# Kernel optimization log

Measured on AMD Instinct MI355X. Metric: run time of the kernel, lower is better.

The kernel has to match this reference:

```python
import jax, jax.numpy as jnp
import numpy as np


def setup_inputs() -> dict:
    key = jax.random.key(0)
    k1, k2, k3, k4, k5 = jax.random.split(key, 5)
    N, T, D, H = 256, 64, 1024, 1024
    x = jax.random.normal(k1, (N, T, D), dtype=jnp.float32)
    A = jax.random.normal(k2, (N, H, 4, 4), dtype=jnp.float32)
    Wx = jax.random.normal(k3, (D, 4 * H), dtype=jnp.float32) / np.sqrt(D)
    Wh = jax.random.normal(k4, (H, 4 * H), dtype=jnp.float32) / np.sqrt(H)
    Wattn = jax.random.normal(k5, (H, 4 * H), dtype=jnp.float32) / np.sqrt(H)
    b = jnp.zeros((4 * H,), dtype=jnp.float32)
    return {"x": x, "A": A, "Wx": Wx, "Wh": Wh, "Wattn": Wattn, "b": b}


def reference(x, A, Wx, Wh, Wattn, b):
    N, T, D = x.shape
    H = A.shape[1]
    A_flat = A.reshape(N, H, 16)           # (N, H, 16) flattened 4x4 grid
    scale = 1.0 / jnp.sqrt(jnp.asarray(H, dtype=x.dtype))

    h0 = A.mean(axis=(2, 3))               # (N, H)
    c0 = h0

    def step(carry, xt):
        prev_h, prev_c = carry
        # scaled dot-product attention over the 16 spatial locations
        scores = jnp.einsum('nh,nhl->nl', prev_h, A_flat) * scale  # (N, 16)
        w = jax.nn.softmax(scores, axis=1)
        attn = jnp.einsum('nhl,nl->nh', A_flat, w)                 # (N, H)
        # fused LSTM gate pre-activation
        a = xt @ Wx + prev_h @ Wh + attn @ Wattn + b               # (N, 4H)
        ai, af, ao, ag = jnp.split(a, 4, axis=1)
        i = jax.nn.sigmoid(ai)
        f = jax.nn.sigmoid(af)
        o = jax.nn.sigmoid(ao)
        g = jnp.tanh(ag)
        next_c = f * prev_c + i * g
        next_h = o * jnp.tanh(next_c)
        return (next_h, next_c), next_h

    xs = jnp.swapaxes(x, 0, 1)             # (T, N, D)
    _, hs = jax.lax.scan(step, (h0, c0), xs)
    return jnp.swapaxes(hs, 0, 1)          # (N, T, H)
```

## Files before the change

kernel.cpp:

```cpp
#include <hip/hip_runtime.h>

typedef _Float16 f16;
typedef _Float16 f16x2 __attribute__((ext_vector_type(2)));
typedef _Float16 f16x4 __attribute__((ext_vector_type(4)));
typedef _Float16 f16x8 __attribute__((ext_vector_type(8)));
typedef float f32x4 __attribute__((ext_vector_type(4)));

#define N_ 256
#define T_ 64
#define D_ 1024
#define H_ 1024
#define K3 3072
#define G4 4096

__global__ void k_transpose(const float* __restrict__ Wx, const float* __restrict__ Wh,
                            const float* __restrict__ Wattn, f16* __restrict__ W3T) {
    __shared__ float tile[32][33];
    int j0 = blockIdx.x * 32;
    int k0 = blockIdx.y * 32;
    int tx = threadIdx.x;
    int ty = threadIdx.y;
    for (int i = 0; i < 4; i++) {
        int k = k0 + ty + i * 8;
        const float* W = (k < 1024) ? Wx : ((k < 2048) ? Wh : Wattn);
        int kr = k & 1023;
        tile[ty + i * 8][tx] = W[(size_t)kr * 4096 + j0 + tx];
    }
    __syncthreads();
    for (int i = 0; i < 4; i++) {
        int j = j0 + ty + i * 8;
        W3T[(size_t)j * K3 + k0 + tx] = (f16)tile[tx][ty + i * 8];
    }
}

__global__ void k_castA(const float* __restrict__ A, f16* __restrict__ A16) {
    int i = blockIdx.x * 256 + threadIdx.x;
    float4 v = ((const float4*)A)[i];
    f16x4 h4 = {(f16)v.x, (f16)v.y, (f16)v.z, (f16)v.w};
    ((f16x4*)A16)[i] = h4;
}

__global__ void k_castX(const float* __restrict__ x, f16* __restrict__ x16) {
    size_t i = (size_t)blockIdx.x * 2048 + (size_t)threadIdx.x * 8;
    float4 v0 = *(const float4*)(x + i);
    float4 v1 = *(const float4*)(x + i + 4);
    f16x8 h;
    h[0] = (f16)v0.x; h[1] = (f16)v0.y; h[2] = (f16)v0.z; h[3] = (f16)v0.w;
    h[4] = (f16)v1.x; h[5] = (f16)v1.y; h[6] = (f16)v1.z; h[7] = (f16)v1.w;
    *(f16x8*)(x16 + i) = h;
}

__global__ void k_castAT(const float* __restrict__ A, f16* __restrict__ AT16) {
    __shared__ f16 sA[16 * 1024];
    int n = blockIdx.x;
    int tid = threadIdx.x;
    for (int i = 0; i < 4; i++) {
        int h = tid + i * 256;
        const float* Ap = A + (size_t)n * 16384 + h * 16;
        float4 v0 = ((const float4*)Ap)[0];
        float4 v1 = ((const float4*)Ap)[1];
        float4 v2 = ((const float4*)Ap)[2];
        float4 v3 = ((const float4*)Ap)[3];
        float vv[16] = {v0.x, v0.y, v0.z, v0.w, v1.x, v1.y, v1.z, v1.w,
                        v2.x, v2.y, v2.z, v2.w, v3.x, v3.y, v3.z, v3.w};
#pragma unroll
        for (int l = 0; l < 16; l++) sA[l * 1024 + h] = (f16)vv[l];
    }
    __syncthreads();
    for (int i = 0; i < 8; i++) {
        int cnk = tid + i * 256;
        f16x8 v = *(const f16x8*)(sA + cnk * 8);
        *(f16x8*)(AT16 + (size_t)n * 16384 + cnk * 8) = v;
    }
}

__global__ __launch_bounds__(512) void k_precompP(
    const f16* __restrict__ AT16, const f16* __restrict__ W3T,
    f16* __restrict__ PT16) {
    int tid = threadIdx.x;
    int wave = tid >> 6;
    int lane = tid & 63;
    int m16 = lane & 15;
    int quad = lane >> 4;
    int bid = blockIdx.x;
    int jb = bid & 31;
    int nb = bid >> 5;
    int j0 = jb * 128 + wave * 16;

    const f16* bp = W3T + (size_t)(j0 + m16) * K3 + 2048 + quad * 8;
    for (int np = 0; np < 16; np++) {
        int n = nb * 32 + np * 2;
        const f16* a0p = AT16 + (size_t)n * 16384 + m16 * 1024 + quad * 8;
        const f16* a1p = a0p + 16384;
        f32x4 ac0 = {0.f, 0.f, 0.f, 0.f};
        f32x4 ac1 = {0.f, 0.f, 0.f, 0.f};
#pragma unroll 4
        for (int ks = 0; ks < 32; ks++) {
            int k = ks * 32;
            f16x8 bb = *(const f16x8*)(bp + k);
            f16x8 a0 = *(const f16x8*)(a0p + k);
            f16x8 a1 = *(const f16x8*)(a1p + k);
            ac0 = __builtin_amdgcn_mfma_f32_16x16x32_f16(a0, bb, ac0, 0, 0, 0);
            ac1 = __builtin_amdgcn_mfma_f32_16x16x32_f16(a1, bb, ac1, 0, 0, 0);
        }
        f16x4 o0 = {(f16)ac0[0], (f16)ac0[1], (f16)ac0[2], (f16)ac0[3]};
        f16x4 o1 = {(f16)ac1[0], (f16)ac1[1], (f16)ac1[2], (f16)ac1[3]};
        *(f16x4*)(PT16 + (size_t)n * 65536 + (size_t)(j0 + m16) * 16 + quad * 4) = o0;
        *(f16x4*)(PT16 + (size_t)(n + 1) * 65536 + (size_t)(j0 + m16) * 16 + quad * 4) = o1;
    }
}

__global__ void k_init(const float* __restrict__ A, f16* __restrict__ Zh,
                       float* __restrict__ c, float* __restrict__ Sc0,
                       float* __restrict__ Sc1, float* __restrict__ Sc2) {
    int n = blockIdx.x;
    int tid = threadIdx.x;
    __shared__ float sred[256][16];
    float s[16];
#pragma unroll
    for (int l = 0; l < 16; l++) s[l] = 0.f;
    for (int i = 0; i < 4; i++) {
        int h = tid + i * 256;
        const float* Ap = A + (size_t)n * 16384 + h * 16;
        float a[16];
        float sum = 0.f;
#pragma unroll
        for (int l = 0; l < 16; l++) { a[l] = Ap[l]; sum += a[l]; }
        float h0 = sum * (1.f / 16.f);
        c[n * 1024 + h] = h0;
        Zh[n * 1024 + h] = (f16)h0;
#pragma unroll
        for (int l = 0; l < 16; l++) s[l] += h0 * a[l];
    }
#pragma unroll
    for (int l = 0; l < 16; l++) sred[tid][l] = s[l];
    __syncthreads();
    for (int st = 128; st > 0; st >>= 1) {
        if (tid < st) {
#pragma unroll
            for (int l = 0; l < 16; l++) sred[tid][l] += sred[tid + st][l];
        }
        __syncthreads();
    }
    if (tid < 16) {
        Sc0[n * 16 + tid] = sred[0][tid];
        Sc1[n * 16 + tid] = 0.f;
        Sc2[n * 16 + tid] = 0.f;
    }
}

__global__ __launch_bounds__(512, 2) void k_step(
    const f16* __restrict__ x16, const f16* __restrict__ W3T,
    const f16* __restrict__ Zin, f16* __restrict__ Zout,
    const f16* __restrict__ A16, const f16* __restrict__ PT16,
    const float* __restrict__ b, float* __restrict__ c,
    const float* __restrict__ Rbuf, float* __restrict__ Wbuf,
    float* __restrict__ Zbuf, float* __restrict__ out, int t) {
    __shared__ float Gs[4][4][64 * 17];
    __shared__ float Hs[64 * 17];
    __shared__ float Ws[64][17];

    int tid = threadIdx.x;
    int wave = tid >> 6;
    int lane = tid & 63;
    int m16 = lane & 15;
    int quad = lane >> 4;
    int bid = blockIdx.x;
    int ht = bid & 63;
    int n0 = (bid >> 6) << 6;
    int hc = ht * 16;

    if (tid < 64) {
        const float* rp = Rbuf + (size_t)(n0 + tid) * 16;
        float4 q0 = ((const float4*)rp)[0];
        float4 q1 = ((const float4*)rp)[1];
        float4 q2 = ((const float4*)rp)[2];
        float4 q3 = ((const float4*)rp)[3];
        float v[16] = {q0.x, q0.y, q0.z, q0.w, q1.x, q1.y, q1.z, q1.w,
                       q2.x, q2.y, q2.z, q2.w, q3.x, q3.y, q3.z, q3.w};
        float mx = -1e30f;
#pragma unroll
        for (int l = 0; l < 16; l++) { v[l] *= 0.03125f; mx = fmaxf(mx, v[l]); }
        float sum = 0.f;
#pragma unroll
        for (int l = 0; l < 16; l++) { v[l] = __expf(v[l] - mx); sum += v[l]; }
        float inv = 1.f / sum;
#pragma unroll
        for (int l = 0; l < 16; l++) Ws[tid][l] = v[l] * inv;
    }
    if (tid < 16) Zbuf[bid * 16 + tid] = 0.f;

    f32x4 acc[4][4];
#pragma unroll
    for (int g = 0; g < 4; g++)
#pragma unroll
        for (int m = 0; m < 4; m++) acc[g][m] = (f32x4){0.f, 0.f, 0.f, 0.f};

    int kb = (wave & 3) * 256;
    const f16* ab;
    size_t aoff[4];
    int bc0;
    if (wave < 4) {
        ab = x16 + (size_t)t * 1024 + kb + quad * 8;
#pragma unroll
        for (int mt = 0; mt < 4; mt++)
            aoff[mt] = (size_t)(n0 + mt * 16 + m16) * (T_ * 1024);
        bc0 = kb;
    } else {
        ab = Zin + kb + quad * 8;
#pragma unroll
        for (int mt = 0; mt < 4; mt++)
            aoff[mt] = (size_t)(n0 + mt * 16 + m16) * 1024;
        bc0 = 1024 + kb;
    }
    const f16* brow[4];
#pragma unroll
    for (int g = 0; g < 4; g++)
        brow[g] = W3T + (size_t)(g * 1024 + hc + m16) * K3 + bc0 + quad * 8;

#pragma unroll 2
    for (int s = 0; s < 8; s++) {
        int k = s * 32;
        f16x8 a[4], bb[4];
#pragma unroll
        for (int mt = 0; mt < 4; mt++) a[mt] = *(const f16x8*)(ab + aoff[mt] + k);
#pragma unroll
        for (int g = 0; g < 4; g++) bb[g] = *(const f16x8*)(brow[g] + k);
#pragma unroll
        for (int g = 0; g < 4; g++)
#pragma unroll
            for (int mt = 0; mt < 4; mt++)
                acc[g][mt] = __builtin_amdgcn_mfma_f32_16x16x32_f16(a[mt], bb[g], acc[g][mt], 0, 0, 0);
    }

    if (wave < 4) {
#pragma unroll
        for (int g = 0; g < 4; g++)
#pragma unroll
            for (int mt = 0; mt < 4; mt++)
#pragma unroll
                for (int r = 0; r < 4; r++)
                    Gs[wave][g][(mt * 16 + quad * 4 + r) * 17 + m16] = acc[g][mt][r];
    }
    __syncthreads();
    if (wave >= 4) {
        int sl = wave - 4;
#pragma unroll
        for (int g = 0; g < 4; g++)
#pragma unroll
            for (int mt = 0; mt < 4; mt++)
#pragma unroll
                for (int r = 0; r < 4; r++)
                    Gs[sl][g][(mt * 16 + quad * 4 + r) * 17 + m16] += acc[g][mt][r];
    }
    __syncthreads();

    {
        int idx0 = tid * 2;
        int nn = idx0 >> 4;
        int hh0 = idx0 & 15;
        int gn = n0 + nn;
        int gh0 = hc + hh0;
        float wv[16];
#pragma unroll
        for (int l = 0; l < 16; l++) wv[l] = Ws[nn][l];
        float att[4][2];
        const f16* pt = PT16 + (size_t)gn * 65536 + (size_t)gh0 * 16;
#pragma unroll
        for (int g = 0; g < 4; g++)
#pragma unroll
            for (int i = 0; i < 2; i++) {
                const f16* p = pt + ((size_t)g * 1024 + i) * 16;
                f16x8 p0 = *(const f16x8*)(p);
                f16x8 p1 = *(const f16x8*)(p + 8);
                float s = 0.f;
#pragma unroll
                for (int l = 0; l < 8; l++)
                    s += (float)p0[l] * wv[l] + (float)p1[l] * wv[l + 8];
                att[g][i] = s;
            }
        float hn2[2];
#pragma unroll
        for (int i = 0; i < 2; i++) {
            int gi = nn * 17 + hh0 + i;
            int gh = gh0 + i;
            float ai = Gs[0][0][gi] + Gs[1][0][gi] + Gs[2][0][gi] + Gs[3][0][gi] + b[gh] + att[0][i];
            float af = Gs[0][1][gi] + Gs[1][1][gi] + Gs[2][1][gi] + Gs[3][1][gi] + b[1024 + gh] + att[1][i];
            float ao = Gs[0][2][gi] + Gs[1][2][gi] + Gs[2][2][gi] + Gs[3][2][gi] + b[2048 + gh] + att[2][i];
            float ag = Gs[0][3][gi] + Gs[1][3][gi] + Gs[2][3][gi] + Gs[3][3][gi] + b[3072 + gh] + att[3][i];
            float ig = 1.f / (1.f + __expf(-ai));
            float fg = 1.f / (1.f + __expf(-af));
            float og = 1.f / (1.f + __expf(-ao));
            float gg = tanhf(ag);
            float cn = fg * c[gn * 1024 + gh] + ig * gg;
            c[gn * 1024 + gh] = cn;
            float hn = og * tanhf(cn);
            hn2[i] = hn;
            Hs[gi] = hn;
        }
        float2 o2 = {hn2[0], hn2[1]};
        *(float2*)(out + ((size_t)gn * T_ + t) * 1024 + gh0) = o2;
        f16x2 z2 = {(f16)hn2[0], (f16)hn2[1]};
        *(f16x2*)(Zout + gn * 1024 + gh0) = z2;
    }
    __syncthreads();

#pragma unroll
    for (int i = 0; i < 2; i++) {
        int idx = i * 512 + tid;
        int nn = idx >> 4;
        int l = idx & 15;
        int gn = n0 + nn;
        const f16* Ap = A16 + (size_t)gn * 16384 + hc * 16 + l;
        float s = 0.f;
#pragma unroll
        for (int hh = 0; hh < 16; hh++)
            s += Hs[nn * 17 + hh] * (float)Ap[hh * 16];
        atomicAdd(Wbuf + gn * 16 + l, s);
    }
}

extern "C" void kernel_launch(void* const* d_in, const int* in_sizes, int n_in,
                              void* d_out, int out_size, void* d_ws, size_t ws_size,
                              hipStream_t stream) {
    const float* x     = (const float*)d_in[0];
    const float* A     = (const float*)d_in[1];
    const float* Wx    = (const float*)d_in[2];
    const float* Wh    = (const float*)d_in[3];
    const float* Wattn = (const float*)d_in[4];
    const float* b     = (const float*)d_in[5];
    float* out = (float*)d_out;

    char* ws = (char*)d_ws;
    size_t off = 0;
    f16* W3T  = (f16*)(ws + off); off += (size_t)G4 * K3 * 2;
    f16* x16  = (f16*)(ws + off); off += (size_t)N_ * T_ * D_ * 2;
    f16* A16  = (f16*)(ws + off); off += (size_t)N_ * H_ * 16 * 2;
    f16* AT16 = (f16*)(ws + off); off += (size_t)N_ * 16 * H_ * 2;
    f16* PT16 = (f16*)(ws + off); off += (size_t)N_ * G4 * 16 * 2;
    f16* Zh0  = (f16*)(ws + off); off += (size_t)N_ * H_ * 2;
    f16* Zh1  = (f16*)(ws + off); off += (size_t)N_ * H_ * 2;
    float* c  = (float*)(ws + off); off += (size_t)N_ * H_ * 4;
    float* Sc0 = (float*)(ws + off); off += (size_t)N_ * 16 * 4;
    float* Sc1 = (float*)(ws + off); off += (size_t)N_ * 16 * 4;
    float* Sc2 = (float*)(ws + off); off += (size_t)N_ * 16 * 4;
    float* Sc[3] = {Sc0, Sc1, Sc2};

    k_transpose<<<dim3(128, 96), dim3(32, 8), 0, stream>>>(Wx, Wh, Wattn, W3T);
    k_castA<<<4096, 256, 0, stream>>>(A, A16);
    k_castX<<<8192, 256, 0, stream>>>(x, x16);
    k_castAT<<<256, 256, 0, stream>>>(A, AT16);
    k_precompP<<<256, 512, 0, stream>>>(AT16, W3T, PT16);
    k_init<<<256, 256, 0, stream>>>(A, Zh0, c, Sc0, Sc1, Sc2);
    for (int t = 0; t < T_; t++) {
        f16* Zin  = (t & 1) ? Zh1 : Zh0;
        f16* Zout = (t & 1) ? Zh0 : Zh1;
        k_step<<<256, 512, 0, stream>>>(x16, W3T, Zin, Zout, A16, PT16, b, c,
                                        Sc[t % 3], Sc[(t + 1) % 3], Sc[(t + 2) % 3],
                                        out, t);
    }
}
```

Before: 2.327 ms.

## Tile precompP through LDS with 8-sample blocks and fuse A cast kernels

Rewrites the P precompute kernel so each block stages an 8-sample slice of transposed A in shared memory and reuses each loaded W fragment across 8 MFMA accumulators. The grid grows from 256 to 1024 blocks for more parallelism. Separately, the standalone A-to-f16 cast kernel is folded into the transposing cast, which removes one launch and one read pass over A. The cost is extra shared memory, barriers and register pressure from 8 accumulators plus 8 cached B fragments.

Measured after the change: 2.020 ms. 1.15x faster.

```diff
diff --git a/kernel.cpp b/kernel.cpp
--- a/kernel.cpp
+++ b/kernel.cpp
@@ -33,13 +33,6 @@
     }
 }
 
-__global__ void k_castA(const float* __restrict__ A, f16* __restrict__ A16) {
-    int i = blockIdx.x * 256 + threadIdx.x;
-    float4 v = ((const float4*)A)[i];
-    f16x4 h4 = {(f16)v.x, (f16)v.y, (f16)v.z, (f16)v.w};
-    ((f16x4*)A16)[i] = h4;
-}
-
 __global__ void k_castX(const float* __restrict__ x, f16* __restrict__ x16) {
     size_t i = (size_t)blockIdx.x * 2048 + (size_t)threadIdx.x * 8;
     float4 v0 = *(const float4*)(x + i);
@@ -50,7 +43,8 @@
     *(f16x8*)(x16 + i) = h;
 }
 
-__global__ void k_castAT(const float* __restrict__ A, f16* __restrict__ AT16) {
+__global__ void k_castAT(const float* __restrict__ A, f16* __restrict__ A16,
+                         f16* __restrict__ AT16) {
     __shared__ f16 sA[16 * 1024];
     int n = blockIdx.x;
     int tid = threadIdx.x;
@@ -63,6 +57,11 @@
         float4 v3 = ((const float4*)Ap)[3];
         float vv[16] = {v0.x, v0.y, v0.z, v0.w, v1.x, v1.y, v1.z, v1.w,
                         v2.x, v2.y, v2.z, v2.w, v3.x, v3.y, v3.z, v3.w};
+        f16x8 lo, hi;
+#pragma unroll
+        for (int l = 0; l < 8; l++) { lo[l] = (f16)vv[l]; hi[l] = (f16)vv[l + 8]; }
+        *(f16x8*)(A16 + (size_t)n * 16384 + h * 16) = lo;
+        *(f16x8*)(A16 + (size_t)n * 16384 + h * 16 + 8) = hi;
 #pragma unroll
         for (int l = 0; l < 16; l++) sA[l * 1024 + h] = (f16)vv[l];
     }
@@ -74,9 +73,10 @@
     }
 }
 
-__global__ __launch_bounds__(512) void k_precompP(
+__global__ __launch_bounds__(512, 4) void k_precompP(
     const f16* __restrict__ AT16, const f16* __restrict__ W3T,
     f16* __restrict__ PT16) {
+    __shared__ f16 As[8 * 16 * 264];
     int tid = threadIdx.x;
     int wave = tid >> 6;
     int lane = tid & 63;
@@ -85,28 +85,46 @@
     int bid = blockIdx.x;
     int jb = bid & 31;
     int nb = bid >> 5;
-    int j0 = jb * 128 + wave * 16;
-
-    const f16* bp = W3T + (size_t)(j0 + m16) * K3 + 2048 + quad * 8;
-    for (int np = 0; np < 16; np++) {
-        int n = nb * 32 + np * 2;
-        const f16* a0p = AT16 + (size_t)n * 16384 + m16 * 1024 + quad * 8;
-        const f16* a1p = a0p + 16384;
-        f32x4 ac0 = {0.f, 0.f, 0.f, 0.f};
-        f32x4 ac1 = {0.f, 0.f, 0.f, 0.f};
-#pragma unroll 4
-        for (int ks = 0; ks < 32; ks++) {
-            int k = ks * 32;
-            f16x8 bb = *(const f16x8*)(bp + k);
-            f16x8 a0 = *(const f16x8*)(a0p + k);
-            f16x8 a1 = *(const f16x8*)(a1p + k);
-            ac0 = __builtin_amdgcn_mfma_f32_16x16x32_f16(a0, bb, ac0, 0, 0, 0);
-            ac1 = __builtin_amdgcn_mfma_f32_16x16x32_f16(a1, bb, ac1, 0, 0, 0);
+    int n0g = nb * 8;
+    int j16 = jb * 128 + wave * 16;
+
+    const f16* bp = W3T + (size_t)(j16 + m16) * K3 + 2048 + quad * 8;
+
+    f32x4 acc[8];
+#pragma unroll
+    for (int n = 0; n < 8; n++) acc[n] = (f32x4){0.f, 0.f, 0.f, 0.f};
+
+    for (int kb = 0; kb < 4; kb++) {
+        __syncthreads();
+        for (int i = 0; i < 8; i++) {
+            int cidx = tid + i * 512;
+            int n  = cidx >> 9;
+            int r  = cidx & 511;
+            int l  = r >> 5;
+            int kc = r & 31;
+            f16x8 v = *(const f16x8*)(AT16 + (size_t)(n0g + n) * 16384 + l * 1024 + kb * 256 + kc * 8);
+            *(f16x8*)(&As[(n * 16 + l) * 264 + kc * 8]) = v;
         }
-        f16x4 o0 = {(f16)ac0[0], (f16)ac0[1], (f16)ac0[2], (f16)ac0[3]};
-        f16x4 o1 = {(f16)ac1[0], (f16)ac1[1], (f16)ac1[2], (f16)ac1[3]};
-        *(f16x4*)(PT16 + (size_t)n * 65536 + (size_t)(j0 + m16) * 16 + quad * 4) = o0;
-        *(f16x4*)(PT16 + (size_t)(n + 1) * 65536 + (size_t)(j0 + m16) * 16 + quad * 4) = o1;
+        __syncthreads();
+        f16x8 bb[8];
+#pragma unroll
+        for (int ks = 0; ks < 8; ks++)
+            bb[ks] = *(const f16x8*)(bp + kb * 256 + ks * 32);
+#pragma unroll
+        for (int n = 0; n < 8; n++) {
+            const f16* ap = &As[(n * 16 + m16) * 264 + quad * 8];
+#pragma unroll
+            for (int ks = 0; ks < 8; ks++) {
+                f16x8 a = *(const f16x8*)(ap + ks * 32);
+                acc[n] = __builtin_amdgcn_mfma_f32_16x16x32_f16(a, bb[ks], acc[n], 0, 0, 0);
+            }
+        }
+    }
+
+#pragma unroll
+    for (int n = 0; n < 8; n++) {
+        f16x4 o = {(f16)acc[n][0], (f16)acc[n][1], (f16)acc[n][2], (f16)acc[n][3]};
+        *(f16x4*)(PT16 + (size_t)(n0g + n) * 65536 + (size_t)(j16 + m16) * 16 + quad * 4) = o;
     }
 }
 
@@ -347,10 +365,9 @@
     float* Sc[3] = {Sc0, Sc1, Sc2};
 
     k_transpose<<<dim3(128, 96), dim3(32, 8), 0, stream>>>(Wx, Wh, Wattn, W3T);
-    k_castA<<<4096, 256, 0, stream>>>(A, A16);
     k_castX<<<8192, 256, 0, stream>>>(x, x16);
-    k_castAT<<<256, 256, 0, stream>>>(A, AT16);
-    k_precompP<<<256, 512, 0, stream>>>(AT16, W3T, PT16);
+    k_castAT<<<256, 256, 0, stream>>>(A, A16, AT16);
+    k_precompP<<<1024, 512, 0, stream>>>(AT16, W3T, PT16);
     k_init<<<256, 256, 0, stream>>>(A, Zh0, c, Sc0, Sc1, Sc2);
     for (int t = 0; t < T_; t++) {
         f16* Zin  = (t & 1) ? Zh1 : Zh0;
```
